# Optimization experiments

Hardware: AMD Instinct MI355X
Metric: run time of the kernel (lower is better)

Reference implementation:

```python
import jax, jax.numpy as jnp
import numpy as np

F, N, C, H, M = 256, 400, 128, 8, 128  # frames, batch*joints, mdl_channels, heads, max_pos
E = C // H


def _layer_norm(z, g, b, eps=1e-5):
    mu = jnp.mean(z, axis=-1, keepdims=True)
    var = jnp.mean((z - mu) ** 2, axis=-1, keepdims=True)
    return (z - mu) * jax.lax.rsqrt(var + eps) * g + b


def setup_inputs() -> dict:
    key = jax.random.key(0)
    ks = jax.random.split(key, 16)
    s = 0.02
    return {
        "x": jax.random.normal(ks[0], (F, N, C), jnp.float32),
        "tree_encoding": jax.random.normal(ks[1], (N, C), jnp.float32),
        "W_qkv": jax.random.normal(ks[2], (3 * C, C), jnp.float32) * s,      # Linear weight (out,in), no bias
        "W_tree_k": jax.random.normal(ks[3], (C, C), jnp.float32) * s,
        "W_tree_v": jax.random.normal(ks[4], (C, C), jnp.float32) * s,
        "emb": jax.random.normal(ks[5], (2 * M + 1, E), jnp.float32) * s,    # distance embedding table
        "W_beta": jax.random.normal(ks[6], (1, 3 * C), jnp.float32) * s,     # lin_beta (out,in), no bias
        "ln1_g": jnp.ones((C,), jnp.float32),
        "ln1_b": jnp.zeros((C,), jnp.float32),
        "ln2_g": jnp.ones((C,), jnp.float32),
        "ln2_b": jnp.zeros((C,), jnp.float32),
        "W1": jax.random.normal(ks[7], (C, C), jnp.float32) * s,
        "b1": jnp.zeros((C,), jnp.float32),
        "W2": jax.random.normal(ks[8], (C, C), jnp.float32) * s,
        "b2": jnp.zeros((C,), jnp.float32),
    }


def reference(x, tree_encoding, W_qkv, W_tree_k, W_tree_v, emb, W_beta,
              ln1_g, ln1_b, ln2_g, ln2_b, W1, b1, W2, b2):
    f, n, c = x.shape
    # qkv projection, no bias
    qkv = x @ W_qkv.T                          # (f, n, 3c)
    q, k, v = jnp.split(qkv, 3, axis=-1)       # each (f, n, c)
    # tree positional encoding added to key/value
    k = k + (tree_encoding @ W_tree_k)[None]
    v = v + (tree_encoding @ W_tree_v)[None]
    # (f, n, c) -> (n, f, h, e): n is the attention batch, f is sequence length
    to_heads = lambda t: t.transpose(1, 0, 2).reshape(n, f, H, E)
    qh, kh, vh = to_heads(q), to_heads(k), to_heads(v)
    # content scores
    qk = jnp.einsum('nlhe,nshe->nhls', qh, kh)
    # relative position bias
    ids = jnp.arange(f)
    dist = jnp.clip(ids[:, None] - ids[None, :], -M, M) + M   # (f, f)
    pe = emb[dist]                                            # (f, f, e)
    qk = qk + jnp.einsum('nlhe,lse->nhls', qh, pe)
    qk = qk + jnp.einsum('nshe,lse->nhls', kh, pe)
    scale = 1.0 / (E ** 0.5)
    att = jax.nn.softmax(qk * scale, axis=-1)                 # (n, h, f, f)
    out = jnp.einsum('nhls,nshe->nlhe', att, vh)              # (n, f, h, e)
    y = out.reshape(n, f, c).transpose(1, 0, 2)               # (f, n, c)
    # gated AddNorm (beta=True): x is residual, y is attention output
    gate = jax.nn.sigmoid(jnp.concatenate([y, x, y - x], axis=-1) @ W_beta.T)
    h1 = _layer_norm(gate * x + (1.0 - gate) * y, ln1_g, ln1_b)
    # FFN (GELU exact, as torch nn.GELU default)
    ff = jax.nn.gelu(h1 @ W1.T + b1, approximate=False) @ W2.T + b2
    return _layer_norm(ff + h1, ln2_g, ln2_b)
```

## Files before the change

kernel.cpp:

```cpp
#include <hip/hip_runtime.h>
#include <math.h>

#define F_DIM 256
#define N_DIM 400
#define C_DIM 128
#define H_DIM 8
#define E_DIM 16
#define ROWS  (F_DIM * N_DIM)
#define SBUF  (N_DIM * H_DIM * F_DIM * E_DIM)

#define S_SCALE 0.6005612043932249f

typedef _Float16 half2_t __attribute__((ext_vector_type(2)));
typedef _Float16 f16x8   __attribute__((ext_vector_type(8)));
typedef float    f32x16  __attribute__((ext_vector_type(16)));
typedef float    f32x4   __attribute__((ext_vector_type(4)));

struct H2x4 { half2_t h[4]; };

__device__ inline f16x8 pack8(float4 a, float4 b) {
    H2x4 t;
    t.h[0] = __builtin_bit_cast(half2_t, __builtin_amdgcn_cvt_pkrtz(a.x, a.y));
    t.h[1] = __builtin_bit_cast(half2_t, __builtin_amdgcn_cvt_pkrtz(a.z, a.w));
    t.h[2] = __builtin_bit_cast(half2_t, __builtin_amdgcn_cvt_pkrtz(b.x, b.y));
    t.h[3] = __builtin_bit_cast(half2_t, __builtin_amdgcn_cvt_pkrtz(b.z, b.w));
    return __builtin_bit_cast(f16x8, t);
}

__device__ inline _Float16 h_rtz(float v) {
    half2_t p = __builtin_bit_cast(half2_t, __builtin_amdgcn_cvt_pkrtz(v, v));
    return p[0];
}

__device__ inline int iclamp256(int v) { return v < 0 ? 0 : (v > 256 ? 256 : v); }

__global__ __launch_bounds__(256) void prep_pack(
    const float* __restrict__ x, const float* __restrict__ Wq,
    const float* __restrict__ emb, const float* __restrict__ te,
    const float* __restrict__ Wtk, const float* __restrict__ Wtv,
    _Float16* __restrict__ xh, _Float16* __restrict__ Wqh,
    _Float16* __restrict__ embh, float* __restrict__ tk, float* __restrict__ tv)
{
    int bid = blockIdx.x;
    int t   = threadIdx.x;
    if (bid < 6400) {
        int i = (bid * 256 + t) * 8;
        const float4* s = (const float4*)(x + i);
        *(uint4*)(xh + i) = __builtin_bit_cast(uint4, pack8(s[0], s[1]));
    } else if (bid < 6424) {
        int i = ((bid - 6400) * 256 + t) * 8;
        const float4* s = (const float4*)(Wq + i);
        *(uint4*)(Wqh + i) = __builtin_bit_cast(uint4, pack8(s[0], s[1]));
    } else if (bid < 6426) {
        int r = (bid - 6424) * 256 + t;
        if (r > 256) return;
        const float4* er = (const float4*)(emb + r * 16);
        float4 e0 = er[0], e1 = er[1], e2 = er[2], e3 = er[3];
        e0.x *= S_SCALE; e0.y *= S_SCALE; e0.z *= S_SCALE; e0.w *= S_SCALE;
        e1.x *= S_SCALE; e1.y *= S_SCALE; e1.z *= S_SCALE; e1.w *= S_SCALE;
        e2.x *= S_SCALE; e2.y *= S_SCALE; e2.z *= S_SCALE; e2.w *= S_SCALE;
        e3.x *= S_SCALE; e3.y *= S_SCALE; e3.z *= S_SCALE; e3.w *= S_SCALE;
        *(uint4*)(embh + r * 16)     = __builtin_bit_cast(uint4, pack8(e0, e1));
        *(uint4*)(embh + r * 16 + 8) = __builtin_bit_cast(uint4, pack8(e2, e3));
    } else {
        int n = bid - 6426;
        const float* W = (t < 128) ? Wtk : Wtv;
        float* outp    = (t < 128) ? tk : tv;
        int j = t & 127;
        float acc = 0.f;
        #pragma unroll 4
        for (int c = 0; c < 128; ++c)
            acc += te[n * 128 + c] * W[c * 128 + j];
        outp[n * 128 + j] = acc;
    }
}

__global__ __launch_bounds__(256) void qkv_gemm(
    const _Float16* __restrict__ xh, const _Float16* __restrict__ Wqh,
    const float* __restrict__ tk, const float* __restrict__ tv,
    _Float16* __restrict__ qn, _Float16* __restrict__ kn, _Float16* __restrict__ vn)
{
    int tid  = threadIdx.x;
    int wave = tid >> 6, lane = tid & 63;
    int m32  = lane & 31, khalf = lane >> 5;
    int row0 = blockIdx.y * 64 + (wave & 1) * 32;
    int col0 = blockIdx.x * 64 + (wave >> 1) * 32;

    const _Float16* xp = xh  + (row0 + m32) * 128 + khalf * 8;
    const _Float16* wp = Wqh + (col0 + m32) * 128 + khalf * 8;

    f32x16 acc;
    #pragma unroll
    for (int i = 0; i < 16; ++i) acc[i] = 0.f;

    #pragma unroll
    for (int k0 = 0; k0 < 128; k0 += 16) {
        f16x8 xa = __builtin_bit_cast(f16x8, *(const uint4*)(xp + k0));
        f16x8 wa = __builtin_bit_cast(f16x8, *(const uint4*)(wp + k0));
        acc = __builtin_amdgcn_mfma_f32_32x32x16_f16(xa, wa, acc, 0, 0, 0);
    }

    int o   = col0 + m32;
    int sec = o >> 7;
    int rem = o & 127;
    #pragma unroll
    for (int reg = 0; reg < 16; ++reg) {
        int r = row0 + (reg & 3) + 8 * (reg >> 2) + 4 * khalf;
        float val = acc[reg];
        if (sec == 0) {
            qn[r * 128 + rem] = h_rtz(val * S_SCALE);
        } else {
            int f = r / 400;
            int n = r - f * 400;
            if (sec == 1) {
                kn[r * 128 + rem] = h_rtz((val + tk[n * 128 + rem]) * S_SCALE);
            } else {
                vn[r * 128 + rem] = (_Float16)(val + tv[n * 128 + rem]);
            }
        }
    }
}

__global__ __launch_bounds__(256) void v_pack(
    const _Float16* __restrict__ vn, _Float16* __restrict__ vT)
{
    __shared__ _Float16 sm[16 * 264];
    int bn = blockIdx.x;
    int n  = bn >> 3, h = bn & 7;
    int t  = threadIdx.x;

    const uint4* src = (const uint4*)(vn + (t * 400 + n) * 128 + h * 16);
    uint4 a = src[0], b = src[1];
    union { uint4 u; _Float16 hv[8]; } ua, ub;
    ua.u = a; ub.u = b;
    #pragma unroll
    for (int e = 0; e < 8; ++e) sm[e * 264 + t]       = ua.hv[e];
    #pragma unroll
    for (int e = 0; e < 8; ++e) sm[(e + 8) * 264 + t] = ub.hv[e];
    __syncthreads();

    #pragma unroll
    for (int k = 0; k < 2; ++k) {
        int idx = (k * 256 + t) * 8;
        int e = idx >> 8, f0 = idx & 255;
        uint4 o = *(const uint4*)(sm + e * 264 + f0);
        *(uint4*)(vT + bn * 4096 + idx) = o;
    }
}

#define R2_STRIDE 258
#define PS_STRIDE 40

__global__ __launch_bounds__(512, 4) void attn_kernel(
    const _Float16* __restrict__ qb, const _Float16* __restrict__ kb,
    const _Float16* __restrict__ vb, const _Float16* __restrict__ embh,
    _Float16* __restrict__ y)
{
    __shared__ __align__(16) _Float16 R2sh[32 * R2_STRIDE];
    __shared__ __align__(16) _Float16 Psh[8 * 32 * PS_STRIDE];

    int tid  = threadIdx.x;
    int wave = tid >> 6, lane = tid & 63;
    int bid  = blockIdx.x;
    int bn   = (bid & 7) * 400 + (bid >> 3);
    int n    = bn >> 3, h = bn & 7;
    int base = bn * 4096;

    int nn  = lane & 31;
    int kh  = lane >> 5;
    int khb = (lane & 32) << 2;
    int cbase = 31 + 4 * kh - nn;
    int dbase = 4 * kh - nn;
    int q16 = (lane >> 4) & 3;

    int nat_off = n * 128 + h * 16 + kh * 8;

    f16x8 aq = __builtin_bit_cast(f16x8,
        *(const uint4*)(qb + (32 * wave + nn) * 51200 + nat_off));

    f16x8 bones;
    #pragma unroll
    for (int i = 0; i < 8; ++i) bones[i] = (_Float16)1.0f;

    f32x4 O[2];
    f32x4 Od[2];
    #pragma unroll
    for (int a = 0; a < 2; ++a)
        #pragma unroll
        for (int r = 0; r < 4; ++r) { O[a][r] = 0.f; Od[a][r] = 0.f; }

    _Float16* psw = Psh + wave * 32 * PS_STRIDE;

    for (int st = 0; st < 8; ++st) {
        f16x8 bk = __builtin_bit_cast(f16x8,
            *(const uint4*)(kb + (32 * st + nn) * 51200 + nat_off));

        for (int ct = wave; ct < 9; ct += 8) {
            int erow = 32 * ct + nn; if (erow > 256) erow = 256;
            f16x8 be = __builtin_bit_cast(f16x8,
                *(const uint4*)(embh + erow * 16 + kh * 8));
            f32x16 c2;
            #pragma unroll
            for (int i = 0; i < 16; ++i) c2[i] = 0.f;
            c2 = __builtin_amdgcn_mfma_f32_32x32x16_f16(bk, be, c2, 0, 0, 0);
            int col = 32 * ct + nn;
            if (col <= 257) {
                #pragma unroll
                for (int r = 0; r < 16; ++r) {
                    int srow = (r & 3) + 8 * (r >> 2) + 4 * kh;
                    R2sh[srow * R2_STRIDE + col] = (_Float16)c2[r];
                }
            }
        }
        __syncthreads();

        f16x8 bv = __builtin_bit_cast(f16x8,
            *(const uint4*)(vb + base + (lane & 15) * 256 + 32 * st + q16 * 8));

        int U0 = 32 * wave - 32 * st + 128;

        f32x16 S;
        #pragma unroll
        for (int i = 0; i < 16; ++i) S[i] = 0.f;
        S = __builtin_amdgcn_mfma_f32_32x32x16_f16(aq, bk, S, 0, 0, 0);

        int br0 = iclamp256(U0 - 31 + nn);
        int br1 = iclamp256(U0 + 1 + nn);
        f16x8 be0 = __builtin_bit_cast(f16x8,
            *(const uint4*)(embh + br0 * 16 + kh * 8));
        f16x8 be1 = __builtin_bit_cast(f16x8,
            *(const uint4*)(embh + br1 * 16 + kh * 8));
        f32x16 W0, W1;
        #pragma unroll
        for (int i = 0; i < 16; ++i) { W0[i] = 0.f; W1[i] = 0.f; }
        W0 = __builtin_amdgcn_mfma_f32_32x32x16_f16(aq, be0, W0, 0, 0, 0);
        W1 = __builtin_amdgcn_mfma_f32_32x32x16_f16(aq, be1, W1, 0, 0, 0);

        half2_t b1p[8];
        #pragma unroll
        for (int r = 0; r < 16; ++r) {
            int rmr = (r & 3) + 8 * (r >> 2);
            int c   = rmr + cbase;
            int addr = ((c & 31) << 2) + khb;
            int w01 = __builtin_bit_cast(int,
                __builtin_amdgcn_cvt_pkrtz(W0[r], W1[r]));
            half2_t hh = __builtin_bit_cast(half2_t,
                __builtin_amdgcn_ds_bpermute(addr, w01));
            b1p[r >> 1][r & 1] = (c < 32) ? hh[0] : hh[1];
        }

        #pragma unroll
        for (int r = 0; r < 16; ++r) {
            int rmr = (r & 3) + 8 * (r >> 2);
            float b1 = (float)b1p[r >> 1][r & 1];
            int d = iclamp256(U0 + rmr + dbase);
            float b2 = (float)R2sh[nn * R2_STRIDE + d];
            float p = __builtin_amdgcn_exp2f(S[r] + b1 + b2);
            int mloc = rmr + 4 * kh;
            psw[mloc * PS_STRIDE + nn] = (_Float16)p;
        }

        #pragma unroll
        for (int a = 0; a < 2; ++a) {
            f16x8 ap = __builtin_bit_cast(f16x8,
                *(const uint4*)(psw + (16 * a + (lane & 15)) * PS_STRIDE + q16 * 8));
            O[a]  = __builtin_amdgcn_mfma_f32_16x16x32_f16(ap, bv,    O[a],  0, 0, 0);
            Od[a] = __builtin_amdgcn_mfma_f32_16x16x32_f16(ap, bones, Od[a], 0, 0, 0);
        }
        __syncthreads();
    }

    #pragma unroll
    for (int a = 0; a < 2; ++a) {
        #pragma unroll
        for (int r = 0; r < 4; ++r) {
            int row  = q16 * 4 + r;
            int lloc = 16 * a + row;
            int lg = 32 * wave + lloc;
            y[(lg * 400 + n) * 128 + h * 16 + (lane & 15)] =
                (_Float16)(O[a][r] / Od[a][r]);
        }
    }
}

__global__ __launch_bounds__(256) void gate_ln1(
    const float* __restrict__ x, const _Float16* __restrict__ yh,
    const float* __restrict__ Wb, const float* __restrict__ g,
    const float* __restrict__ b, float* __restrict__ h1)
{
    int tid  = threadIdx.x;
    int r    = blockIdx.x * 4 + (tid >> 6);
    int lane = tid & 63;
    int c    = lane * 2;

    float2 xv = *(const float2*)(x + r * 128 + c);
    half2_t yv2 = *(const half2_t*)(yh + r * 128 + c);
    float yvx = (float)yv2[0], yvy = (float)yv2[1];
    float2 w0 = *(const float2*)(Wb + c);
    float2 w1 = *(const float2*)(Wb + 128 + c);
    float2 w2 = *(const float2*)(Wb + 256 + c);

    float sv = yvx * w0.x + yvy * w0.y
             + xv.x * w1.x + xv.y * w1.y
             + (yvx - xv.x) * w2.x + (yvy - xv.y) * w2.y;
    #pragma unroll
    for (int off = 32; off > 0; off >>= 1) sv += __shfl_xor(sv, off);
    float gate = 1.0f / (1.0f + __expf(-sv));

    float z0 = gate * xv.x + (1.0f - gate) * yvx;
    float z1 = gate * xv.y + (1.0f - gate) * yvy;
    float s1 = z0 + z1, s2 = z0 * z0 + z1 * z1;
    #pragma unroll
    for (int off = 32; off > 0; off >>= 1) {
        s1 += __shfl_xor(s1, off);
        s2 += __shfl_xor(s2, off);
    }
    float mu  = s1 * (1.0f / 128.0f);
    float var = s2 * (1.0f / 128.0f) - mu * mu;
    float rs  = rsqrtf(var + 1e-5f);

    float2 gv = *(const float2*)(g + c);
    float2 bv = *(const float2*)(b + c);
    float2 ov;
    ov.x = (z0 - mu) * rs * gv.x + bv.x;
    ov.y = (z1 - mu) * rs * gv.y + bv.y;
    *(float2*)(h1 + r * 128 + c) = ov;
}

__global__ __launch_bounds__(256) void ff1_gemm(
    const float* __restrict__ A, const float* __restrict__ W,
    const float* __restrict__ bias, _Float16* __restrict__ outp)
{
    int tid  = threadIdx.x;
    int wave = tid >> 6, lane = tid & 63;
    int m32  = lane & 31, khalf = lane >> 5;
    int row0 = blockIdx.y * 64 + (wave & 1) * 32;
    int col0 = blockIdx.x * 64 + (wave >> 1) * 32;

    const float* ap = A + (row0 + m32) * 128 + khalf * 8;
    const float* wp = W + (col0 + m32) * 128 + khalf * 8;

    f32x16 acc;
    #pragma unroll
    for (int i = 0; i < 16; ++i) acc[i] = 0.f;

    #pragma unroll
    for (int k0 = 0; k0 < 128; k0 += 16) {
        float4 aa = *(const float4*)(ap + k0);
        float4 ab = *(const float4*)(ap + k0 + 4);
        float4 wa = *(const float4*)(wp + k0);
        float4 wb = *(const float4*)(wp + k0 + 4);
        acc = __builtin_amdgcn_mfma_f32_32x32x16_f16(pack8(aa, ab), pack8(wa, wb), acc, 0, 0, 0);
    }

    int   c  = col0 + m32;
    float bi = bias[c];
    #pragma unroll
    for (int reg = 0; reg < 16; ++reg) {
        int r = row0 + (reg & 3) + 8 * (reg >> 2) + 4 * khalf;
        float v = acc[reg] + bi;
        v = 0.5f * v * (1.0f + erff(v * 0.70710678118654752f));
        outp[r * 128 + c] = (_Float16)v;
    }
}

__global__ __launch_bounds__(256) void ff2_ln2(
    const _Float16* __restrict__ A, const float* __restrict__ W2,
    const float* __restrict__ b2, const float* __restrict__ h1,
    const float* __restrict__ g, const float* __restrict__ bb,
    float* __restrict__ outp)
{
    __shared__ float Cs[32 * 132];
    int tid  = threadIdx.x;
    int wave = tid >> 6, lane = tid & 63;
    int m32  = lane & 31, khalf = lane >> 5;
    int row0 = blockIdx.x * 32;
    int col0 = wave * 32;

    const _Float16* ap = A  + (row0 + m32) * 128 + khalf * 8;
    const float*    wp = W2 + (col0 + m32) * 128 + khalf * 8;

    f32x16 acc;
    #pragma unroll
    for (int i = 0; i < 16; ++i) acc[i] = 0.f;

    #pragma unroll
    for (int k0 = 0; k0 < 128; k0 += 16) {
        f16x8 aa16 = __builtin_bit_cast(f16x8, *(const uint4*)(ap + k0));
        float4 wa = *(const float4*)(wp + k0);
        float4 wb = *(const float4*)(wp + k0 + 4);
        acc = __builtin_amdgcn_mfma_f32_32x32x16_f16(aa16, pack8(wa, wb), acc, 0, 0, 0);
    }

    #pragma unroll
    for (int reg = 0; reg < 16; ++reg) {
        int rloc = (reg & 3) + 8 * (reg >> 2) + 4 * khalf;
        Cs[rloc * 132 + col0 + m32] = acc[reg];
    }
    __syncthreads();

    int rloc = tid >> 3, seg = (tid & 7) * 16;
    int r = row0 + rloc;
    float z[16];
    float s1 = 0.f, s2 = 0.f;
    #pragma unroll
    for (int j4 = 0; j4 < 4; ++j4) {
        float4 cv = *(const float4*)(Cs + rloc * 132 + seg + j4 * 4);
        float4 hv = *(const float4*)(h1 + r * 128 + seg + j4 * 4);
        float4 bv = *(const float4*)(b2 + seg + j4 * 4);
        z[j4*4+0] = cv.x + bv.x + hv.x;
        z[j4*4+1] = cv.y + bv.y + hv.y;
        z[j4*4+2] = cv.z + bv.z + hv.z;
        z[j4*4+3] = cv.w + bv.w + hv.w;
        s1 += z[j4*4+0] + z[j4*4+1] + z[j4*4+2] + z[j4*4+3];
        s2 += z[j4*4+0]*z[j4*4+0] + z[j4*4+1]*z[j4*4+1]
            + z[j4*4+2]*z[j4*4+2] + z[j4*4+3]*z[j4*4+3];
    }
    #pragma unroll
    for (int off = 4; off > 0; off >>= 1) {
        s1 += __shfl_xor(s1, off);
        s2 += __shfl_xor(s2, off);
    }
    float mu  = s1 * (1.0f / 128.0f);
    float var = s2 * (1.0f / 128.0f) - mu * mu;
    float rs  = rsqrtf(var + 1e-5f);
    #pragma unroll
    for (int j4 = 0; j4 < 4; ++j4) {
        float4 gv = *(const float4*)(g  + seg + j4 * 4);
        float4 bv = *(const float4*)(bb + seg + j4 * 4);
        float4 ov;
        ov.x = (z[j4*4+0] - mu) * rs * gv.x + bv.x;
        ov.y = (z[j4*4+1] - mu) * rs * gv.y + bv.y;
        ov.z = (z[j4*4+2] - mu) * rs * gv.z + bv.z;
        ov.w = (z[j4*4+3] - mu) * rs * gv.w + bv.w;
        *(float4*)(outp + r * 128 + seg + j4 * 4) = ov;
    }
}

extern "C" void kernel_launch(void* const* d_in, const int* in_sizes, int n_in,
                              void* d_out, int out_size, void* d_ws, size_t ws_size,
                              hipStream_t stream)
{
    const float* x     = (const float*)d_in[0];
    const float* te    = (const float*)d_in[1];
    const float* Wqkv  = (const float*)d_in[2];
    const float* Wtk   = (const float*)d_in[3];
    const float* Wtv   = (const float*)d_in[4];
    const float* emb   = (const float*)d_in[5];
    const float* Wbeta = (const float*)d_in[6];
    const float* ln1g  = (const float*)d_in[7];
    const float* ln1b  = (const float*)d_in[8];
    const float* ln2g  = (const float*)d_in[9];
    const float* ln2b  = (const float*)d_in[10];
    const float* W1    = (const float*)d_in[11];
    const float* b1    = (const float*)d_in[12];
    const float* W2    = (const float*)d_in[13];
    const float* b2    = (const float*)d_in[14];
    float* outp = (float*)d_out;

    float* ws = (float*)d_ws;
    float* tk = ws;
    float* tv = ws + 51200;
    float* qb_region = ws + 102400;
    float* kb_region = qb_region + SBUF;
    float* vb_region = kb_region + SBUF;
    float* yb        = vb_region + SBUF;

    _Float16* qnat = (_Float16*)qb_region;
    _Float16* knat = (_Float16*)kb_region;
    _Float16* vnat = (_Float16*)vb_region;
    _Float16* vT   = (_Float16*)(vb_region + SBUF / 2);
    _Float16* embh = (_Float16*)(qb_region + SBUF / 2);
    _Float16* yh   = (_Float16*)yb;
    _Float16* xh   = (_Float16*)(kb_region + SBUF / 2);
    _Float16* Wqh  = (_Float16*)(yb + SBUF / 2);

    float*    h1   = kb_region;
    _Float16* ff1h = (_Float16*)qb_region;

    prep_pack<<<6826, 256, 0, stream>>>(x, Wqkv, emb, te, Wtk, Wtv,
                                        xh, Wqh, embh, tk, tv);
    qkv_gemm<<<dim3(6, 1600), 256, 0, stream>>>(xh, Wqh, tk, tv, qnat, knat, vnat);
    v_pack<<<3200, 256, 0, stream>>>(vnat, vT);
    attn_kernel<<<3200, 512, 0, stream>>>(qnat, knat, vT, embh, yh);
    gate_ln1<<<ROWS / 4, 256, 0, stream>>>(x, yh, Wbeta, ln1g, ln1b, h1);
    ff1_gemm<<<dim3(2, 1600), 256, 0, stream>>>(h1, W1, b1, ff1h);
    ff2_ln2<<<3200, 256, 0, stream>>>(ff1h, W2, b2, h1, ln2g, ln2b, outp);
}
```

Baseline: 525.8 us.

## Remap GEMM blocks per XCD, store fp16 h1 for FF1, spread R2 tile

The QKV and FF1 GEMMs switch to a 1D grid whose block index is remapped so that consecutive blocks on the same XCD share row panels, which is meant to improve L2 reuse. gate_ln1 now also writes an fp16 copy of h1, and ff1_gemm reads that copy instead of converting fp32 activations, halving its activation reads. In the attention kernel, the ninth R2 tile is rotated across waves each step instead of always going to wave 0, which balances the work. The price is an extra fp16 write in gate_ln1.

```diff
diff --git a/kernel.cpp b/kernel.cpp
--- a/kernel.cpp
+++ b/kernel.cpp
@@ -83,8 +83,14 @@
     int tid  = threadIdx.x;
     int wave = tid >> 6, lane = tid & 63;
     int m32  = lane & 31, khalf = lane >> 5;
-    int row0 = blockIdx.y * 64 + (wave & 1) * 32;
-    int col0 = blockIdx.x * 64 + (wave >> 1) * 32;
+
+    int bid = blockIdx.x;
+    int xcd = bid & 7;
+    int tt  = bid >> 3;
+    int cb  = tt % 6;
+    int rp  = (tt / 6) * 8 + xcd;
+    int row0 = rp * 64 + (wave & 1) * 32;
+    int col0 = cb * 64 + (wave >> 1) * 32;
 
     const _Float16* xp = xh  + (row0 + m32) * 128 + khalf * 8;
     const _Float16* wp = Wqh + (col0 + m32) * 128 + khalf * 8;
@@ -195,7 +201,7 @@
         f16x8 bk = __builtin_bit_cast(f16x8,
             *(const uint4*)(kb + (32 * st + nn) * 51200 + nat_off));
 
-        for (int ct = wave; ct < 9; ct += 8) {
+        auto r2tile = [&](int ct) {
             int erow = 32 * ct + nn; if (erow > 256) erow = 256;
             f16x8 be = __builtin_bit_cast(f16x8,
                 *(const uint4*)(embh + erow * 16 + kh * 8));
@@ -204,14 +210,16 @@
             for (int i = 0; i < 16; ++i) c2[i] = 0.f;
             c2 = __builtin_amdgcn_mfma_f32_32x32x16_f16(bk, be, c2, 0, 0, 0);
             int col = 32 * ct + nn;
-            if (col <= 257) {
+            if (col <= 256) {
                 #pragma unroll
                 for (int r = 0; r < 16; ++r) {
                     int srow = (r & 3) + 8 * (r >> 2) + 4 * kh;
                     R2sh[srow * R2_STRIDE + col] = (_Float16)c2[r];
                 }
             }
-        }
+        };
+        r2tile(wave);
+        if (wave == (st & 7)) r2tile(8);
         __syncthreads();
 
         f16x8 bv = __builtin_bit_cast(f16x8,
@@ -286,7 +294,8 @@
 __global__ __launch_bounds__(256) void gate_ln1(
     const float* __restrict__ x, const _Float16* __restrict__ yh,
     const float* __restrict__ Wb, const float* __restrict__ g,
-    const float* __restrict__ b, float* __restrict__ h1)
+    const float* __restrict__ b, float* __restrict__ h1,
+    _Float16* __restrict__ h1h)
 {
     int tid  = threadIdx.x;
     int r    = blockIdx.x * 4 + (tid >> 6);
@@ -325,20 +334,28 @@
     ov.x = (z0 - mu) * rs * gv.x + bv.x;
     ov.y = (z1 - mu) * rs * gv.y + bv.y;
     *(float2*)(h1 + r * 128 + c) = ov;
+    *(uint*)(h1h + r * 128 + c) = __builtin_bit_cast(uint,
+        __builtin_amdgcn_cvt_pkrtz(ov.x, ov.y));
 }
 
 __global__ __launch_bounds__(256) void ff1_gemm(
-    const float* __restrict__ A, const float* __restrict__ W,
+    const _Float16* __restrict__ A, const float* __restrict__ W,
     const float* __restrict__ bias, _Float16* __restrict__ outp)
 {
     int tid  = threadIdx.x;
     int wave = tid >> 6, lane = tid & 63;
     int m32  = lane & 31, khalf = lane >> 5;
-    int row0 = blockIdx.y * 64 + (wave & 1) * 32;
-    int col0 = blockIdx.x * 64 + (wave >> 1) * 32;
-
-    const float* ap = A + (row0 + m32) * 128 + khalf * 8;
-    const float* wp = W + (col0 + m32) * 128 + khalf * 8;
+
+    int bid = blockIdx.x;
+    int xcd = bid & 7;
+    int tt  = bid >> 3;
+    int cb  = tt & 1;
+    int rp  = (tt >> 1) * 8 + xcd;
+    int row0 = rp * 64 + (wave & 1) * 32;
+    int col0 = cb * 64 + (wave >> 1) * 32;
+
+    const _Float16* ap = A + (row0 + m32) * 128 + khalf * 8;
+    const float*    wp = W + (col0 + m32) * 128 + khalf * 8;
 
     f32x16 acc;
     #pragma unroll
@@ -346,11 +363,10 @@
 
     #pragma unroll
     for (int k0 = 0; k0 < 128; k0 += 16) {
-        float4 aa = *(const float4*)(ap + k0);
-        float4 ab = *(const float4*)(ap + k0 + 4);
+        f16x8 aa16 = __builtin_bit_cast(f16x8, *(const uint4*)(ap + k0));
         float4 wa = *(const float4*)(wp + k0);
         float4 wb = *(const float4*)(wp + k0 + 4);
-        acc = __builtin_amdgcn_mfma_f32_32x32x16_f16(pack8(aa, ab), pack8(wa, wb), acc, 0, 0, 0);
+        acc = __builtin_amdgcn_mfma_f32_32x32x16_f16(aa16, pack8(wa, wb), acc, 0, 0, 0);
     }
 
     int   c  = col0 + m32;
@@ -476,14 +492,15 @@
     _Float16* Wqh  = (_Float16*)(yb + SBUF / 2);
 
     float*    h1   = kb_region;
+    _Float16* h1h  = (_Float16*)vb_region;
     _Float16* ff1h = (_Float16*)qb_region;
 
     prep_pack<<<6826, 256, 0, stream>>>(x, Wqkv, emb, te, Wtk, Wtv,
                                         xh, Wqh, embh, tk, tv);
-    qkv_gemm<<<dim3(6, 1600), 256, 0, stream>>>(xh, Wqh, tk, tv, qnat, knat, vnat);
+    qkv_gemm<<<9600, 256, 0, stream>>>(xh, Wqh, tk, tv, qnat, knat, vnat);
     v_pack<<<3200, 256, 0, stream>>>(vnat, vT);
     attn_kernel<<<3200, 512, 0, stream>>>(qnat, knat, vT, embh, yh);
-    gate_ln1<<<ROWS / 4, 256, 0, stream>>>(x, yh, Wbeta, ln1g, ln1b, h1);
-    ff1_gemm<<<dim3(2, 1600), 256, 0, stream>>>(h1, W1, b1, ff1h);
+    gate_ln1<<<ROWS / 4, 256, 0, stream>>>(x, yh, Wbeta, ln1g, ln1b, h1, h1h);
+    ff1_gemm<<<3200, 256, 0, stream>>>(h1h, W1, b1, ff1h);
     ff2_ln2<<<3200, 256, 0, stream>>>(ff1h, W2, b2, h1, ln2g, ln2b, outp);
 }
```

Result: no change. 519.2 us (-1.3%).
